# Kernel tuning notes

Measured on AMD Instinct MI355X. Metric: run time of the kernel, lower is better.

Reference implementation:

```python
import jax, jax.numpy as jnp
import numpy as np

N_WAY = 5
K_SHOT = 5
TEMPERATURE = 1.0
NEG = -1e9  # emulates 'column does not exist' for pad columns beyond umask_length
EPS = 1e-12  # matches torch F.normalize eps


def _l2n(x, axis):
    n = jnp.sqrt(jnp.sum(x * x, axis=axis, keepdims=True))
    return x / jnp.maximum(n, EPS)


def setup_inputs() -> dict:
    key = jax.random.key(0)
    k1, k2, k3, k4, k5 = jax.random.split(key, 5)
    b, c, h, w = 4, 64, 5, 5
    q, u = 75, 100
    support_xf = jax.random.normal(k1, (b, N_WAY * K_SHOT, c, h, w), jnp.float32)
    query_xf = jax.random.normal(k2, (b, q, c, h, w), jnp.float32)
    unlabeled_xf = jax.random.normal(k3, (b, u, c, h, w), jnp.float32)
    support_y = jax.random.randint(k4, (b, N_WAY * K_SHOT), 0, N_WAY)
    query_y = jax.random.randint(k5, (b, q), 0, N_WAY)
    return {"support_xf": support_xf, "support_y": support_y, "query_xf": query_xf,
            "query_y": query_y, "unlabeled_xf": unlabeled_xf}


def _forward(support_xf, query_xf, unlabeled_xf, query_y):
    b, q, c, h, w = query_xf.shape
    M_s = K_SHOT * h * w
    unl = unlabeled_xf.reshape(b, -1, c, h, w)
    u = unl.shape[1]
    M_u = u * h * w
    # pooled unlabeled local descriptors, flattened in (u, h, w) order -> [b, c, M_u]
    unl_feat = unl.transpose(0, 2, 1, 3, 4).reshape(b, c, M_u)
    # support -> [b, n_way, c, k_shot*h*w]
    sup = support_xf.reshape(b, N_WAY, K_SHOT, c, h, w).transpose(0, 1, 3, 2, 4, 5).reshape(b, N_WAY, c, M_s)
    # cosine similarity unlabeled -> support: [b, n_way, M_u, M_s]
    u2s = jnp.einsum('bwcn,bcm->bwmn', _l2n(sup, 2), _l2n(unl_feat, 1))
    pool = u2s.transpose(0, 2, 1, 3).reshape(b, M_u, N_WAY * M_s)
    s_nearest = jnp.argmax(pool, axis=1)          # per support loc: nearest unlabeled loc
    u_nearest = jnp.argmax(pool, axis=2)          # per unlabeled loc: nearest support loc
    mutual = jnp.take_along_axis(s_nearest, u_nearest, axis=1) == jnp.arange(M_u)[None, :]  # [b, M_u]
    # class with max similarity per unlabeled location
    cls = jnp.argmax(jnp.max(u2s, axis=-1), axis=1)  # [b, M_u]
    umask = jax.nn.one_hot(cls, N_WAY, dtype=jnp.float32).transpose(0, 2, 1) \
            * mutual[:, None, :].astype(jnp.float32)  # [b, n_way, M_u]
    counts = umask.sum(-1)                          # [b, n_way]
    L = counts.max()                                # umask_length (traced)
    # stream compaction via stable argsort of the 0/1 mask (preserves original order)
    order = jnp.argsort(-umask, axis=-1)            # jnp.argsort is stable
    pts = unl_feat.transpose(0, 2, 1)               # [b, M_u, c]
    gath = jnp.take_along_axis(pts[:, None, :, :], order[..., None], axis=2)  # [b, n_way, M_u, c]
    valid = (jnp.arange(M_u)[None, None, :] < counts[:, :, None]).astype(jnp.float32)
    comp = gath * valid[..., None]                  # rows beyond count are zeros (as in torch)
    s_cat = jnp.concatenate([sup, comp.transpose(0, 1, 3, 2)], axis=-1)  # [b, n_way, c, M_s+M_u]
    M_tot = M_s + M_u
    qn = _l2n(query_xf.reshape(b, q, c, h * w), 2)
    scn = _l2n(s_cat, 2)
    sim = jnp.einsum('bqcm,bwcn->bqwmn', qn, scn)   # [b, q, n_way, M_q, M_tot]
    sim = (sim + 1.0) * 0.5                          # FourLayer_64F branch
    # columns beyond umask_length don't exist in the torch dense tensor -> exclude from maxes
    pad = jnp.arange(M_tot)[None, None, None, None, :] >= (M_s + L)
    sim = jnp.where(pad, NEG, sim)
    M_q = h * w
    qm = sim.transpose(0, 1, 3, 2, 4).reshape(b, q, M_q, N_WAY * M_tot)
    support_nearest = jnp.argmax(qm, axis=2)        # [b, q, n_way*M_tot]
    query_nearest = jnp.argmax(qm, axis=3)          # [b, q, M_q]
    g = jnp.take_along_axis(support_nearest, query_nearest, axis=2)
    q_mask = (g == jnp.arange(M_q)[None, None, :]).astype(sim.dtype)  # mutual NN mask
    query_value = (jnp.max(sim, axis=-1) * q_mask[:, :, None, :]).sum(-1)  # [b, q, n_way]
    logits = query_value.reshape(b * q, N_WAY) / TEMPERATURE
    y = query_y.reshape(b * q)
    logp = jax.nn.log_softmax(logits, axis=-1)
    loss = -jnp.take_along_axis(logp, y[:, None], axis=1).mean()
    return loss


def reference(support_xf, support_y, query_xf, query_y, unlabeled_xf):
    return _forward(support_xf, query_xf, unlabeled_xf, query_y)
```

## Files before the change

kernel.cpp:

```cpp
#include <hip/hip_runtime.h>

#define NEGINF (-1e30f)

constexpr size_t OF_UNL  = 0;
constexpr size_t OF_SUP  = OF_UNL  + (size_t)4*2500*64;
constexpr size_t OF_SUPT = OF_SUP  + (size_t)4*5*125*64;
constexpr size_t OF_QT   = OF_SUPT + (size_t)4*5*64*128;
constexpr size_t OF_ROWV = OF_QT   + (size_t)300*64*25;
constexpr size_t OF_ROWI = OF_ROWV + (size_t)4*5*8*2500;
constexpr size_t OF_CVI  = OF_ROWI + (size_t)4*5*8*2500;
constexpr size_t OF_CMP  = OF_CVI  + (size_t)4*5*125*20*2;
constexpr size_t OF_CNT  = OF_CMP  + (size_t)4*5*2500;
constexpr size_t OF_UNEAR= OF_CNT  + 20;
constexpr size_t OF_SNEAR= OF_UNEAR+ 10000;
constexpr size_t OF_BV   = OF_SNEAR+ 2500;
constexpr size_t OF_BP   = OF_BV   + 37500;
constexpr size_t OF_AMX  = OF_BP   + 37500;

__global__ __launch_bounds__(256) void knorm(
    const float* __restrict__ sup, const float* __restrict__ qry,
    const float* __restrict__ unl,
    float* __restrict__ unl_n, float* __restrict__ sup_n,
    float* __restrict__ supT, float* __restrict__ qt)
{
    int gid = blockIdx.x * 256 + threadIdx.x;
    int loc = gid >> 4;
    int sub = gid & 15;
    if (loc >= 20000) return;

    const float* src;
    float* dst1; int dstr1;
    float* dst2 = nullptr;

    if (loc < 10000) {
        int b = loc / 2500, m = loc % 2500;
        int u = m / 25, hw = m % 25;
        src  = unl + ((size_t)(b*100 + u) * 64) * 25 + hw;
        dst1 = unl_n + (size_t)loc * 64; dstr1 = 1;
    } else if (loc < 12500) {
        int idx = loc - 10000;
        int b = idx / 625, r = idx % 625;
        int w = r / 125,  n = r % 125;
        int shot = n / 25, hw = n % 25;
        src  = sup + ((size_t)(b*25 + w*5 + shot) * 64) * 25 + hw;
        dst1 = sup_n + (size_t)idx * 64; dstr1 = 1;
        dst2 = supT + ((size_t)(b*5 + w) * 64) * 128 + n;
    } else {
        int idx = loc - 12500;
        int bq = idx / 25, mq = idx % 25;
        src  = qry + ((size_t)bq * 64) * 25 + mq;
        dst1 = qt + ((size_t)bq * 64) * 25 + mq; dstr1 = 25;
    }

    float v[4]; float ss = 0.f;
    int c0 = sub * 4;
#pragma unroll
    for (int j = 0; j < 4; ++j) { v[j] = src[(size_t)(c0 + j) * 25]; ss += v[j] * v[j]; }
#pragma unroll
    for (int msk = 1; msk < 16; msk <<= 1) ss += __shfl_xor(ss, msk);
    float sc = 1.f / fmaxf(sqrtf(ss), 1e-12f);
#pragma unroll
    for (int j = 0; j < 4; ++j) {
        float o = v[j] * sc;
        dst1[(size_t)(c0 + j) * dstr1] = o;
        if (dst2) dst2[(size_t)(c0 + j) * 128] = o;
    }
}

__global__ __launch_bounds__(256) void kb(
    const float* __restrict__ unl_n, const float* __restrict__ supT,
    float* __restrict__ rowv, int* __restrict__ rowi, float* __restrict__ colvi)
{
    int bid = blockIdx.x;
    int nc = bid & 3;
    int mb = (bid >> 2) % 20;
    int bw = bid / 80;
    int b  = bw / 5;
    int tid = threadIdx.x;
    int lane = tid & 63, wv = tid >> 6;

    __shared__ float uls[128 * 65];
    __shared__ float sls[64 * 36];
    __shared__ float sv_[4][32];
    __shared__ int   si_[4][32];

    int m0 = mb * 128;
    int n0 = nc * 32;

    for (int i = tid; i < 128 * 16; i += 256) {
        int row = i >> 4, c4 = (i & 15) * 4;
        int m = m0 + row;
        float4 x = make_float4(0.f, 0.f, 0.f, 0.f);
        if (m < 2500) x = *(const float4*)(unl_n + ((size_t)(b * 2500 + m)) * 64 + c4);
        uls[row * 65 + c4 + 0] = x.x;
        uls[row * 65 + c4 + 1] = x.y;
        uls[row * 65 + c4 + 2] = x.z;
        uls[row * 65 + c4 + 3] = x.w;
    }
    {
        int c = tid >> 2, q = tid & 3;
        const float* sp = supT + ((size_t)bw * 64 + c) * 128 + n0 + q * 8;
        float4 a = *(const float4*)sp;
        float4 d4 = *(const float4*)(sp + 4);
        float* d = &sls[c * 36 + q * 8];
        d[0] = a.x; d[1] = a.y; d[2] = a.z; d[3] = a.w;
        d[4] = d4.x; d[5] = d4.y; d[6] = d4.z; d[7] = d4.w;
    }
    __syncthreads();

    int ml = tid & 127;
    int m  = m0 + ml;
    int nh = tid >> 7;
    int nbase = nh * 16;
    int nn_total = (125 - n0) < 32 ? (125 - n0) : 32;
    const float* myrow = &uls[ml * 65];

    float acc[16];
#pragma unroll
    for (int j = 0; j < 16; ++j) acc[j] = 0.f;

    for (int c = 0; c < 64; ++c) {
        float uv = myrow[c];
        const float4* sr = (const float4*)&sls[c * 36 + nbase];
        float4 s0 = sr[0], s1 = sr[1], s2 = sr[2], s3 = sr[3];
        acc[0]  = fmaf(uv, s0.x, acc[0]);  acc[1]  = fmaf(uv, s0.y, acc[1]);
        acc[2]  = fmaf(uv, s0.z, acc[2]);  acc[3]  = fmaf(uv, s0.w, acc[3]);
        acc[4]  = fmaf(uv, s1.x, acc[4]);  acc[5]  = fmaf(uv, s1.y, acc[5]);
        acc[6]  = fmaf(uv, s1.z, acc[6]);  acc[7]  = fmaf(uv, s1.w, acc[7]);
        acc[8]  = fmaf(uv, s2.x, acc[8]);  acc[9]  = fmaf(uv, s2.y, acc[9]);
        acc[10] = fmaf(uv, s2.z, acc[10]); acc[11] = fmaf(uv, s2.w, acc[11]);
        acc[12] = fmaf(uv, s3.x, acc[12]); acc[13] = fmaf(uv, s3.y, acc[13]);
        acc[14] = fmaf(uv, s3.z, acc[14]); acc[15] = fmaf(uv, s3.w, acc[15]);
    }

    int nnloc = nn_total - nbase;
    nnloc = nnloc < 0 ? 0 : (nnloc > 16 ? 16 : nnloc);
    float rbv = NEGINF; int rbi = 0;
    for (int j = 0; j < nnloc; ++j)
        if (acc[j] > rbv) { rbv = acc[j]; rbi = n0 + nbase + j; }
    if (m < 2500) {
        int ck = nc * 2 + nh;
        rowv[((size_t)bw * 8 + ck) * 2500 + m] = rbv;
        rowi[((size_t)bw * 8 + ck) * 2500 + m] = rbi;
    }

#pragma unroll
    for (int j = 0; j < 16; ++j) {
        float v = (m < 2500 && (nbase + j) < nn_total) ? acc[j] : NEGINF;
        float vm = v;
#pragma unroll
        for (int s2 = 1; s2 < 64; s2 <<= 1) vm = fmaxf(vm, __shfl_xor(vm, s2));
        unsigned long long msk = __ballot(v == vm);
        int first = __ffsll((unsigned long long)msk) - 1;
        if (lane == 0) { sv_[wv][nbase + j] = vm; si_[wv][nbase + j] = m0 + (wv & 1) * 64 + first; }
    }
    __syncthreads();
    if (tid < nn_total) {
        int w0 = (tid < 16) ? 0 : 2;
        float v = sv_[w0][tid];     int vi = si_[w0][tid];
        float v2 = sv_[w0 + 1][tid]; int i2 = si_[w0 + 1][tid];
        if (v2 > v || (v2 == v && i2 < vi)) { v = v2; vi = i2; }
        float* cv = colvi + ((((size_t)bw) * 125 + (n0 + tid)) * 20 + mb) * 2;
        cv[0] = v; ((int*)cv)[1] = vi;
    }
}

__global__ __launch_bounds__(256) void kmerge(
    const float* __restrict__ rowv, const int* __restrict__ rowi,
    const float* __restrict__ colvi,
    int* __restrict__ unear, int* __restrict__ snear)
{
    int it = blockIdx.x * 256 + threadIdx.x;
    if (it < 10000) {
        int b = it / 2500, m = it % 2500;
        float bv = NEGINF; int bi = 0;
#pragma unroll
        for (int w = 0; w < 5; ++w) {
#pragma unroll
            for (int ck = 0; ck < 8; ++ck) {
                size_t o = (((size_t)(b * 5 + w)) * 8 + ck) * 2500 + m;
                float v = rowv[o];
                if (v > bv) { bv = v; bi = w * 125 + rowi[o]; }
            }
        }
        unear[it] = bi;
    } else if (it < 12500) {
        int idx = it - 10000;
        const float* p = colvi + (size_t)idx * 40;
        float bv = NEGINF; int bi = 0x7fffffff;
        for (int mb2 = 0; mb2 < 20; ++mb2) {
            float v = p[mb2 * 2]; int vi = ((const int*)p)[mb2 * 2 + 1];
            if (v > bv || (v == bv && vi < bi)) { bv = v; bi = vi; }
        }
        snear[idx] = bi;
    }
}

__global__ __launch_bounds__(256) void kcmp(
    const int* __restrict__ unear, const int* __restrict__ snear,
    int* __restrict__ cmp, int* __restrict__ cntg)
{
    int p = blockIdx.x;
    int b = p / 5, way = p % 5;
    int tid = threadIdx.x, lane = tid & 63, wv = tid >> 6;
    __shared__ unsigned long long masks[40];
    __shared__ int base[40];

    for (int ch = wv; ch < 40; ch += 4) {
        int m = ch * 64 + lane;
        bool ok = false;
        if (m < 2500) {
            int un = unear[b * 2500 + m];
            ok = (un / 125 == way) && (snear[b * 625 + un] == m);
        }
        unsigned long long msk = __ballot(ok ? 1 : 0);
        if (lane == 0) masks[ch] = msk;
    }
    __syncthreads();
    if (tid == 0) {
        int s = 0;
        for (int ch = 0; ch < 40; ++ch) { base[ch] = s; s += __popcll(masks[ch]); }
        cntg[p] = s;
    }
    __syncthreads();
    for (int ch = wv; ch < 40; ch += 4) {
        unsigned long long msk = masks[ch];
        if ((msk >> lane) & 1ull) {
            int pre = __popcll(msk & ((1ull << lane) - 1ull));
            cmp[(size_t)p * 2500 + base[ch] + pre] = ch * 64 + lane;
        }
    }
}

__global__ __launch_bounds__(256) void kc1(
    const float* __restrict__ qt, const float* __restrict__ sup_n,
    const float* __restrict__ unl_n, const int* __restrict__ cmp,
    const int* __restrict__ cntg,
    float* __restrict__ bvg, int* __restrict__ bpg,
    unsigned char* __restrict__ amaxg)
{
    int bid = blockIdx.x;
    int w = bid % 5, bq = bid / 5;
    int b = bq / 75;
    int tid = threadIdx.x;

    const float* qtb = qt + (size_t)bq * 64 * 25;

    int L = 0;
#pragma unroll
    for (int i = 0; i < 20; ++i) { int v = cntg[i]; L = L > v ? L : v; }
    int cntw = 0, wb = 0;
#pragma unroll
    for (int w2 = 0; w2 < 5; ++w2) {
        int c2 = cntg[b * 5 + w2];
        if (w2 < w) wb += 125 + c2;
        if (w2 == w) cntw = c2;
    }
    int cw = 125 + cntw;

    __shared__ float simb[25 * 257];
    __shared__ float redv[8][25];
    __shared__ int   redp[8][25];

    int rg = tid / 25, rq = tid % 25;
    float bv1 = NEGINF; int bp1 = 0x7fffffff;

    for (int c0 = 0; c0 < cw; c0 += 256) {
        int n = c0 + tid;
        if (n < cw) {
            const float* colp;
            if (n < 125) colp = sup_n + (((size_t)(b * 5 + w)) * 125 + n) * 64;
            else {
                int m = cmp[((size_t)(b * 5 + w)) * 2500 + (n - 125)];
                colp = unl_n + ((size_t)(b * 2500 + m)) * 64;
            }
            float acc[25];
#pragma unroll
            for (int i = 0; i < 25; ++i) acc[i] = 0.f;
            for (int c = 0; c < 64; c += 4) {
                float4 cv = *(const float4*)(colp + c);
                const float* qr = qtb + c * 25;
#pragma unroll
                for (int mq = 0; mq < 25; ++mq) {
                    acc[mq] = fmaf(cv.x, qr[mq],      acc[mq]);
                    acc[mq] = fmaf(cv.y, qr[25 + mq], acc[mq]);
                    acc[mq] = fmaf(cv.z, qr[50 + mq], acc[mq]);
                    acc[mq] = fmaf(cv.w, qr[75 + mq], acc[mq]);
                }
            }
            float cmax = NEGINF; int cam = 0;
#pragma unroll
            for (int mq = 0; mq < 25; ++mq) {
                float s = (acc[mq] + 1.0f) * 0.5f;
                if (s > cmax) { cmax = s; cam = mq; }
                simb[mq * 257 + tid] = s;
            }
            amaxg[(size_t)bq * 3200 + (wb + n)] = (unsigned char)cam;
        }
        __syncthreads();
        if (tid < 200) {
            int base = rg * 32;
            for (int i = 0; i < 32; ++i) {
                int n2 = c0 + base + i;
                if (n2 < cw) {
                    float s = simb[rq * 257 + base + i];
                    if (s > bv1) { bv1 = s; bp1 = ((w * 2625 + n2) << 12) | (wb + n2); }
                }
            }
        }
        __syncthreads();
    }

    if (tid < 200) { redv[rg][rq] = bv1; redp[rg][rq] = bp1; }
    __syncthreads();
    if (tid < 25) {
        float v = redv[0][tid]; int p = redp[0][tid];
#pragma unroll
        for (int g = 1; g < 8; ++g)
            if (redv[g][tid] > v) { v = redv[g][tid]; p = redp[g][tid]; }
        if (L > cntw) {
            int pp = ((w * 2625 + 125 + cntw) << 12) | 0xFFF;
            if (0.5f > v || (0.5f == v && pp < p)) { v = 0.5f; p = pp; }
        }
        size_t o = ((size_t)bq * 5 + w) * 25 + tid;
        bvg[o] = v; bpg[o] = p;
    }
}

__global__ __launch_bounds__(64) void kce(
    const float* __restrict__ bvg, const int* __restrict__ bpg,
    const unsigned char* __restrict__ amaxg, const int* __restrict__ qy,
    float* __restrict__ out)
{
    int bq = blockIdx.x;
    int tid = threadIdx.x;
    __shared__ float qmask[25];
    __shared__ float lg[5];
    if (tid < 25) {
        float v = NEGINF; int p = 0x7fffffff;
#pragma unroll
        for (int w = 0; w < 5; ++w) {
            size_t o = ((size_t)bq * 5 + w) * 25 + tid;
            float v2 = bvg[o]; int p2 = bpg[o];
            if (v2 > v || (v2 == v && p2 < p)) { v = v2; p = p2; }
        }
        int pos = p & 0xFFF;
        int g = (pos == 0xFFF) ? 0 : (int)amaxg[(size_t)bq * 3200 + pos];
        qmask[tid] = (g == tid) ? 1.0f : 0.0f;
    }
    __syncthreads();
    if (tid < 5) {
        float s = 0.f;
#pragma unroll
        for (int mq = 0; mq < 25; ++mq)
            s += bvg[((size_t)bq * 5 + tid) * 25 + mq] * qmask[mq];
        lg[tid] = s;
    }
    __syncthreads();
    if (tid == 0) {
        int y = qy[bq];
        float mx = lg[0];
#pragma unroll
        for (int w = 1; w < 5; ++w) mx = fmaxf(mx, lg[w]);
        float se = 0.f;
#pragma unroll
        for (int w = 0; w < 5; ++w) se += expf(lg[w] - mx);
        float loss = -(lg[y] - mx - logf(se));
        atomicAdd(out, loss * (1.0f / 300.0f));
    }
}

extern "C" void kernel_launch(void* const* d_in, const int* in_sizes, int n_in,
                              void* d_out, int out_size, void* d_ws, size_t ws_size,
                              hipStream_t stream)
{
    const float* sup = (const float*)d_in[0];
    const float* qry = (const float*)d_in[2];
    const int*   qy  = (const int*)d_in[3];
    const float* unl = (const float*)d_in[4];

    float* ws    = (float*)d_ws;
    float* unl_n = ws + OF_UNL;
    float* sup_n = ws + OF_SUP;
    float* supT  = ws + OF_SUPT;
    float* qt    = ws + OF_QT;
    float* rowv  = ws + OF_ROWV;
    int*   rowi  = (int*)(ws + OF_ROWI);
    float* colvi = ws + OF_CVI;
    int*   cmp   = (int*)(ws + OF_CMP);
    int*   cntg  = (int*)(ws + OF_CNT);
    int*   unear = (int*)(ws + OF_UNEAR);
    int*   snear = (int*)(ws + OF_SNEAR);
    float* bvg   = ws + OF_BV;
    int*   bpg   = (int*)(ws + OF_BP);
    unsigned char* amaxg = (unsigned char*)(ws + OF_AMX);

    hipMemsetAsync(d_out, 0, sizeof(float), stream);

    hipLaunchKernelGGL(knorm, dim3(1250), dim3(256), 0, stream,
                       sup, qry, unl, unl_n, sup_n, supT, qt);
    hipLaunchKernelGGL(kb, dim3(1600), dim3(256), 0, stream,
                       unl_n, supT, rowv, rowi, colvi);
    hipLaunchKernelGGL(kmerge, dim3(49), dim3(256), 0, stream,
                       rowv, rowi, colvi, unear, snear);
    hipLaunchKernelGGL(kcmp, dim3(20), dim3(256), 0, stream,
                       unear, snear, cmp, cntg);
    hipLaunchKernelGGL(kc1, dim3(1500), dim3(256), 0, stream,
                       qt, sup_n, unl_n, cmp, cntg, bvg, bpg, amaxg);
    hipLaunchKernelGGL(kce, dim3(300), dim3(64), 0, stream,
                       bvg, bpg, amaxg, qy, (float*)d_out);
}
```

Baseline: 181.9 us.

## Restructure kc1 to tile columns in LDS and broadcast query rows via scalar loads

The query-vs-column similarity kernel now stages 64 columns at a time in shared memory and splits the 25 query rows across four waves (7 rows each). Query rows are fetched with inline-asm scalar loads from a new row-major, zero-padded query layout that knorm now writes. Row maxima move from a shared-memory scan to wave shuffles and ballots, and the per-column argmax is merged across waves. kmerge is also relaunched with 64-thread blocks for more parallelism. The change aims to cut per-thread register pressure and redundant global query reads, at the cost of more synchronisation and fragile inline assembly.

```diff
diff --git a/kernel.cpp b/kernel.cpp
--- a/kernel.cpp
+++ b/kernel.cpp
@@ -6,7 +6,7 @@
 constexpr size_t OF_SUP  = OF_UNL  + (size_t)4*2500*64;
 constexpr size_t OF_SUPT = OF_SUP  + (size_t)4*5*125*64;
 constexpr size_t OF_QT   = OF_SUPT + (size_t)4*5*64*128;
-constexpr size_t OF_ROWV = OF_QT   + (size_t)300*64*25;
+constexpr size_t OF_ROWV = OF_QT   + (size_t)300*28*64;
 constexpr size_t OF_ROWI = OF_ROWV + (size_t)4*5*8*2500;
 constexpr size_t OF_CVI  = OF_ROWI + (size_t)4*5*8*2500;
 constexpr size_t OF_CMP  = OF_CVI  + (size_t)4*5*125*20*2;
@@ -24,9 +24,18 @@
     float* __restrict__ supT, float* __restrict__ qt)
 {
     int gid = blockIdx.x * 256 + threadIdx.x;
+    if (gid >= 320000) {
+        int t = gid - 320000;
+        if (t < 14400) {
+            int bq = t / 48, r = t % 48;
+            int row = 25 + r / 16, ch = r % 16;
+            *(float4*)(qt + ((size_t)bq * 28 + row) * 64 + ch * 4) =
+                make_float4(0.f, 0.f, 0.f, 0.f);
+        }
+        return;
+    }
     int loc = gid >> 4;
     int sub = gid & 15;
-    if (loc >= 20000) return;
 
     const float* src;
     float* dst1; int dstr1;
@@ -49,7 +58,7 @@
         int idx = loc - 12500;
         int bq = idx / 25, mq = idx % 25;
         src  = qry + ((size_t)bq * 64) * 25 + mq;
-        dst1 = qt + ((size_t)bq * 64) * 25 + mq; dstr1 = 25;
+        dst1 = qt + ((size_t)bq * 28 + mq) * 64; dstr1 = 1;
     }
 
     float v[4]; float ss = 0.f;
@@ -165,12 +174,12 @@
     }
 }
 
-__global__ __launch_bounds__(256) void kmerge(
+__global__ __launch_bounds__(64) void kmerge(
     const float* __restrict__ rowv, const int* __restrict__ rowi,
     const float* __restrict__ colvi,
     int* __restrict__ unear, int* __restrict__ snear)
 {
-    int it = blockIdx.x * 256 + threadIdx.x;
+    int it = blockIdx.x * 64 + threadIdx.x;
     if (it < 10000) {
         int b = it / 2500, m = it % 2500;
         float bv = NEGINF; int bi = 0;
@@ -232,6 +241,37 @@
     }
 }
 
+typedef __attribute__((ext_vector_type(4))) float f4s;
+
+#define QLOAD(CG, Q0,Q1,Q2,Q3,Q4,Q5,Q6) \
+  asm volatile( \
+    "s_load_dwordx4 %0, %[b], %c[o0]\n\t" \
+    "s_load_dwordx4 %1, %[b], %c[o1]\n\t" \
+    "s_load_dwordx4 %2, %[b], %c[o2]\n\t" \
+    "s_load_dwordx4 %3, %[b], %c[o3]\n\t" \
+    "s_load_dwordx4 %4, %[b], %c[o4]\n\t" \
+    "s_load_dwordx4 %5, %[b], %c[o5]\n\t" \
+    "s_load_dwordx4 %6, %[b], %c[o6]\n\t" \
+    "s_waitcnt lgkmcnt(0)" \
+    : "=s"(Q0), "=s"(Q1), "=s"(Q2), "=s"(Q3), "=s"(Q4), "=s"(Q5), "=s"(Q6) \
+    : [b]"s"(qbp), \
+      [o0]"i"((CG)*16 + 0*256), [o1]"i"((CG)*16 + 1*256), \
+      [o2]"i"((CG)*16 + 2*256), [o3]"i"((CG)*16 + 3*256), \
+      [o4]"i"((CG)*16 + 4*256), [o5]"i"((CG)*16 + 5*256), \
+      [o6]"i"((CG)*16 + 6*256))
+
+#define CGSTEP(CG) { \
+    f4s q0,q1,q2,q3,q4,q5,q6; \
+    QLOAD(CG, q0,q1,q2,q3,q4,q5,q6); \
+    float4 cl = *(const float4*)&cls[lane * 68 + (CG) * 4]; \
+    acc[0]=fmaf(q0.x,cl.x,fmaf(q0.y,cl.y,fmaf(q0.z,cl.z,fmaf(q0.w,cl.w,acc[0])))); \
+    acc[1]=fmaf(q1.x,cl.x,fmaf(q1.y,cl.y,fmaf(q1.z,cl.z,fmaf(q1.w,cl.w,acc[1])))); \
+    acc[2]=fmaf(q2.x,cl.x,fmaf(q2.y,cl.y,fmaf(q2.z,cl.z,fmaf(q2.w,cl.w,acc[2])))); \
+    acc[3]=fmaf(q3.x,cl.x,fmaf(q3.y,cl.y,fmaf(q3.z,cl.z,fmaf(q3.w,cl.w,acc[3])))); \
+    acc[4]=fmaf(q4.x,cl.x,fmaf(q4.y,cl.y,fmaf(q4.z,cl.z,fmaf(q4.w,cl.w,acc[4])))); \
+    acc[5]=fmaf(q5.x,cl.x,fmaf(q5.y,cl.y,fmaf(q5.z,cl.z,fmaf(q5.w,cl.w,acc[5])))); \
+    acc[6]=fmaf(q6.x,cl.x,fmaf(q6.y,cl.y,fmaf(q6.z,cl.z,fmaf(q6.w,cl.w,acc[6])))); }
+
 __global__ __launch_bounds__(256) void kc1(
     const float* __restrict__ qt, const float* __restrict__ sup_n,
     const float* __restrict__ unl_n, const int* __restrict__ cmp,
@@ -243,8 +283,9 @@
     int w = bid % 5, bq = bid / 5;
     int b = bq / 75;
     int tid = threadIdx.x;
-
-    const float* qtb = qt + (size_t)bq * 64 * 25;
+    int lane = tid & 63;
+    int wvu = __builtin_amdgcn_readfirstlane(tid >> 6);
+    int pbw = b * 5 + w;
 
     int L = 0;
 #pragma unroll
@@ -258,66 +299,98 @@
     }
     int cw = 125 + cntw;
 
-    __shared__ float simb[25 * 257];
-    __shared__ float redv[8][25];
-    __shared__ int   redp[8][25];
-
-    int rg = tid / 25, rq = tid % 25;
-    float bv1 = NEGINF; int bp1 = 0x7fffffff;
-
-    for (int c0 = 0; c0 < cw; c0 += 256) {
-        int n = c0 + tid;
+    __shared__ float cls[64 * 68];
+    __shared__ float amxv[4][64];
+    __shared__ int   amxg_[4][64];
+    __shared__ float redv[25];
+    __shared__ int   redn[25];
+
+    const float* qbp = qt + ((size_t)bq * 28 + wvu * 7) * 64;
+
+    float rv[7]; int rn[7];
+#pragma unroll
+    for (int j = 0; j < 7; ++j) { rv[j] = NEGINF; rn[j] = 0x7fffffff; }
+
+    int nb = (cw + 63) >> 6;
+
+    for (int b4 = 0; b4 < nb; ++b4) {
+        if (b4 > 0 && tid < 64) {
+            int n = (b4 - 1) * 64 + tid;
+            if (n < cw) {
+                float v = amxv[0][tid]; int g = amxg_[0][tid];
+#pragma unroll
+                for (int g2 = 1; g2 < 4; ++g2)
+                    if (amxv[g2][tid] > v) { v = amxv[g2][tid]; g = amxg_[g2][tid]; }
+                amaxg[(size_t)bq * 3200 + (wb + n)] = (unsigned char)g;
+            }
+        }
+#pragma unroll
+        for (int k = 0; k < 4; ++k) {
+            int i = tid + k * 256;
+            int row = i >> 4, ch = i & 15;
+            int n = b4 * 64 + row;
+            float4 x = make_float4(0.f, 0.f, 0.f, 0.f);
+            if (n < cw) {
+                const float* cp;
+                if (n < 125) cp = sup_n + (((size_t)pbw) * 125 + n) * 64;
+                else { int m = cmp[((size_t)pbw) * 2500 + (n - 125)];
+                       cp = unl_n + ((size_t)(b * 2500 + m)) * 64; }
+                x = *(const float4*)(cp + ch * 4);
+            }
+            *(float4*)&cls[row * 68 + ch * 4] = x;
+        }
+        __syncthreads();
+
+        float acc[7];
+#pragma unroll
+        for (int j = 0; j < 7; ++j) acc[j] = 0.f;
+
+        CGSTEP(0);  CGSTEP(1);  CGSTEP(2);  CGSTEP(3);
+        CGSTEP(4);  CGSTEP(5);  CGSTEP(6);  CGSTEP(7);
+        CGSTEP(8);  CGSTEP(9);  CGSTEP(10); CGSTEP(11);
+        CGSTEP(12); CGSTEP(13); CGSTEP(14); CGSTEP(15);
+
+        bool colvalid = (b4 * 64 + lane) < cw;
+        float cmax = NEGINF; int cam = 0;
+#pragma unroll
+        for (int j = 0; j < 7; ++j) {
+            int mq = wvu * 7 + j;
+            float s = (acc[j] + 1.0f) * 0.5f;
+            float sm = (colvalid && mq < 25) ? s : NEGINF;
+            if (sm > cmax) { cmax = sm; cam = mq; }
+            float vm = sm;
+#pragma unroll
+            for (int t = 1; t < 64; t <<= 1) vm = fmaxf(vm, __shfl_xor(vm, t));
+            unsigned long long msk = __ballot(sm == vm);
+            int first = __ffsll(msk) - 1;
+            if (vm > rv[j]) { rv[j] = vm; rn[j] = b4 * 64 + first; }
+        }
+        amxv[wvu][lane] = cmax; amxg_[wvu][lane] = cam;
+        __syncthreads();
+    }
+
+    if (tid < 64) {
+        int n = (nb - 1) * 64 + tid;
         if (n < cw) {
-            const float* colp;
-            if (n < 125) colp = sup_n + (((size_t)(b * 5 + w)) * 125 + n) * 64;
-            else {
-                int m = cmp[((size_t)(b * 5 + w)) * 2500 + (n - 125)];
-                colp = unl_n + ((size_t)(b * 2500 + m)) * 64;
-            }
-            float acc[25];
-#pragma unroll
-            for (int i = 0; i < 25; ++i) acc[i] = 0.f;
-            for (int c = 0; c < 64; c += 4) {
-                float4 cv = *(const float4*)(colp + c);
-                const float* qr = qtb + c * 25;
-#pragma unroll
-                for (int mq = 0; mq < 25; ++mq) {
-                    acc[mq] = fmaf(cv.x, qr[mq],      acc[mq]);
-                    acc[mq] = fmaf(cv.y, qr[25 + mq], acc[mq]);
-                    acc[mq] = fmaf(cv.z, qr[50 + mq], acc[mq]);
-                    acc[mq] = fmaf(cv.w, qr[75 + mq], acc[mq]);
-                }
-            }
-            float cmax = NEGINF; int cam = 0;
-#pragma unroll
-            for (int mq = 0; mq < 25; ++mq) {
-                float s = (acc[mq] + 1.0f) * 0.5f;
-                if (s > cmax) { cmax = s; cam = mq; }
-                simb[mq * 257 + tid] = s;
-            }
-            amaxg[(size_t)bq * 3200 + (wb + n)] = (unsigned char)cam;
-        }
-        __syncthreads();
-        if (tid < 200) {
-            int base = rg * 32;
-            for (int i = 0; i < 32; ++i) {
-                int n2 = c0 + base + i;
-                if (n2 < cw) {
-                    float s = simb[rq * 257 + base + i];
-                    if (s > bv1) { bv1 = s; bp1 = ((w * 2625 + n2) << 12) | (wb + n2); }
-                }
-            }
-        }
-        __syncthreads();
-    }
-
-    if (tid < 200) { redv[rg][rq] = bv1; redp[rg][rq] = bp1; }
-    __syncthreads();
+            float v = amxv[0][tid]; int g = amxg_[0][tid];
+#pragma unroll
+            for (int g2 = 1; g2 < 4; ++g2)
+                if (amxv[g2][tid] > v) { v = amxv[g2][tid]; g = amxg_[g2][tid]; }
+            amaxg[(size_t)bq * 3200 + (wb + n)] = (unsigned char)g;
+        }
+    }
+    if (lane == 0) {
+#pragma unroll
+        for (int j = 0; j < 7; ++j) {
+            int mq = wvu * 7 + j;
+            if (mq < 25) { redv[mq] = rv[j]; redn[mq] = rn[j]; }
+        }
+    }
+    __syncthreads();
+
     if (tid < 25) {
-        float v = redv[0][tid]; int p = redp[0][tid];
-#pragma unroll
-        for (int g = 1; g < 8; ++g)
-            if (redv[g][tid] > v) { v = redv[g][tid]; p = redp[g][tid]; }
+        float v = redv[tid]; int nn = redn[tid];
+        int p = ((w * 2625 + nn) << 12) | (wb + nn);
         if (L > cntw) {
             int pp = ((w * 2625 + 125 + cntw) << 12) | 0xFFF;
             if (0.5f > v || (0.5f == v && pp < p)) { v = 0.5f; p = pp; }
@@ -397,11 +470,11 @@
 
     hipMemsetAsync(d_out, 0, sizeof(float), stream);
 
-    hipLaunchKernelGGL(knorm, dim3(1250), dim3(256), 0, stream,
+    hipLaunchKernelGGL(knorm, dim3(1307), dim3(256), 0, stream,
                        sup, qry, unl, unl_n, sup_n, supT, qt);
     hipLaunchKernelGGL(kb, dim3(1600), dim3(256), 0, stream,
                        unl_n, supT, rowv, rowi, colvi);
-    hipLaunchKernelGGL(kmerge, dim3(49), dim3(256), 0, stream,
+    hipLaunchKernelGGL(kmerge, dim3(196), dim3(64), 0, stream,
                        rowv, rowi, colvi, unear, snear);
     hipLaunchKernelGGL(kcmp, dim3(20), dim3(256), 0, stream,
                        unear, snear, cmp, cntg);
```

After: 183.1 us. No clear change (+0.7%).
